# Kernel tuning notes

Measured on AMD Instinct MI355X. Metric: run time of the kernel, lower is better.

## Reference

```python
import jax, jax.numpy as jnp
import numpy as np

D_V, D_Q, D_H = 256, 128, 64

def setup_inputs() -> dict:
    key = jax.random.key(0)
    ks = jax.random.split(key, 8)
    B, T = 512, 512
    query = jax.random.normal(ks[0], (B, D_Q), dtype=jnp.float32)
    values = jax.random.normal(ks[1], (B, T, D_V), dtype=jnp.float32)
    s1 = 1.0 / np.sqrt(D_V)
    s2 = 1.0 / np.sqrt(D_Q)
    sv = 1.0 / np.sqrt(D_H)
    W1 = jax.random.uniform(ks[2], (D_H, D_V), jnp.float32, -s1, s1)
    b1 = jax.random.uniform(ks[3], (D_H,), jnp.float32, -s1, s1)
    W2 = jax.random.uniform(ks[4], (D_H, D_Q), jnp.float32, -s2, s2)
    b2 = jax.random.uniform(ks[5], (D_H,), jnp.float32, -s2, s2)
    Wv = jax.random.uniform(ks[6], (1, D_H), jnp.float32, -sv, sv)
    bv = jax.random.uniform(ks[7], (1,), jnp.float32, -sv, sv)
    return {"query": query, "values": values, "W1": W1, "b1": b1,
            "W2": W2, "b2": b2, "Wv": Wv, "bv": bv}

def reference(query, values, W1, b1, W2, b2, Wv, bv):
    # hidden_with_time_axis: [B,1,128]
    h = jnp.einsum('btv,hv->bth', values, W1) + b1 \
        + (jnp.einsum('bq,hq->bh', query, W2) + b2)[:, None, :]   # [B,T,64]
    score = jnp.einsum('bth,oh->bto', jnp.tanh(h), Wv) + bv        # [B,T,1]
    attention_weights = jax.nn.softmax(score, axis=0)              # softmax over dim 0, as written
    context_vector = jnp.sum(attention_weights * values, axis=0)   # [T,256]
    return (context_vector, attention_weights)
```

## Files before the change

### kernel.cpp

```cpp
#include <hip/hip_runtime.h>
#include <hip/hip_bf16.h>

#define Tt 512
#define Bb 512
#define DV 256
#define DQ 128
#define DH 64
#define CTXN (Tt * DV)

typedef __attribute__((ext_vector_type(8))) short bf16x8;
typedef __attribute__((ext_vector_type(4))) float f32x4;

__device__ __forceinline__ unsigned short f2bf(float x) {
  unsigned u = __float_as_uint(x);
  u += 0x7FFFu + ((u >> 16) & 1u);
  return (unsigned short)(u >> 16);
}

__global__ void qh_kernel(const float* __restrict__ query,
                          const float* __restrict__ W2,
                          const float* __restrict__ b1,
                          const float* __restrict__ b2,
                          float* __restrict__ qh) {
  int b = blockIdx.x;
  int h = threadIdx.x;
  __shared__ float q[DQ];
  q[h]      = query[b * DQ + h];
  q[h + 64] = query[b * DQ + h + 64];
  __syncthreads();
  const float* w2r = W2 + h * DQ;
  float acc = 0.f;
#pragma unroll 8
  for (int k = 0; k < DQ; ++k) acc = fmaf(w2r[k], q[k], acc);
  qh[b * DH + h] = acc + b1[h] + b2[h];
}

__global__ void w1_cvt_kernel(const float* __restrict__ W1,
                              unsigned short* __restrict__ w1bf) {
  int i = blockIdx.x * 256 + threadIdx.x;
  w1bf[i] = f2bf(W1[i]);
}

__global__ __launch_bounds__(256, 2) void score_kernel(
    const float* __restrict__ values,
    const unsigned short* __restrict__ w1bf,
    const float* __restrict__ qh,
    const float* __restrict__ Wv,
    const float* __restrict__ bv,
    float* __restrict__ sT) {
  __shared__ __align__(16) unsigned short lA[64 * DV];
  __shared__ __align__(16) unsigned short lB[DH * DV];
  const int tid = threadIdx.x;
  const int m0 = blockIdx.x * 64;
  const int bidx = m0 >> 9;

  const uint4* w1v = (const uint4*)w1bf;
#pragma unroll
  for (int i = 0; i < 8; ++i) {
    int vec = i * 256 + tid;
    uint4 d = w1v[vec];
    int row = vec >> 5;
    int u = vec & 31;
    int byte = (row << 9) + (u << 4);
    *(uint4*)((char*)lB + (byte ^ ((row & 7) << 4))) = d;
  }
  const float4* vg = (const float4*)values + m0 * (DV / 4);
#pragma unroll
  for (int i = 0; i < 16; ++i) {
    int vec = i * 256 + tid;
    float4 d = vg[vec];
    int row = vec >> 6;
    int c4 = vec & 63;
    uint2 p;
    p.x = (unsigned)f2bf(d.x) | ((unsigned)f2bf(d.y) << 16);
    p.y = (unsigned)f2bf(d.z) | ((unsigned)f2bf(d.w) << 16);
    int byte = (row << 9) + (c4 << 3);
    *(uint2*)((char*)lA + (byte ^ ((row & 7) << 4))) = p;
  }
  __syncthreads();

  const int wv = tid >> 6;
  const int lane = tid & 63;
  const int lrow = lane & 15;
  const int g = lane >> 4;

  f32x4 acc[4];
#pragma unroll
  for (int nt = 0; nt < 4; ++nt) acc[nt] = (f32x4){0.f, 0.f, 0.f, 0.f};

  const int arow = wv * 16 + lrow;
#pragma unroll
  for (int ks = 0; ks < 8; ++ks) {
    int k2 = (ks * 32 + g * 8) * 2;
    int abyte = ((arow << 9) + k2) ^ ((arow & 7) << 4);
    bf16x8 af = *(const bf16x8*)((const char*)lA + abyte);
#pragma unroll
    for (int nt = 0; nt < 4; ++nt) {
      int brow = nt * 16 + lrow;
      bf16x8 bf = *(const bf16x8*)((const char*)lB +
                                   (((brow << 9) + k2) ^ ((brow & 7) << 4)));
      acc[nt] = __builtin_amdgcn_mfma_f32_16x16x32_bf16(af, bf, acc[nt], 0, 0, 0);
    }
  }

  float bv0 = bv[0];
  float sc[4] = {0.f, 0.f, 0.f, 0.f};
#pragma unroll
  for (int nt = 0; nt < 4; ++nt) {
    int col = nt * 16 + lrow;
    float qv = qh[bidx * DH + col];
    float wvc = Wv[col];
#pragma unroll
    for (int j = 0; j < 4; ++j) {
      float hv = acc[nt][j] + qv;
      float e = __expf(2.f * hv);
      float th = (e - 1.f) / (e + 1.f);
      sc[j] = fmaf(th, wvc, sc[j]);
    }
  }
#pragma unroll
  for (int j = 0; j < 4; ++j) {
    float v = sc[j];
    v += __shfl_xor(v, 1);
    v += __shfl_xor(v, 2);
    v += __shfl_xor(v, 4);
    v += __shfl_xor(v, 8);
    sc[j] = v;
  }
  if (lrow == 0) {
#pragma unroll
    for (int j = 0; j < 4; ++j) {
      int m = m0 + wv * 16 + g * 4 + j;
      int tt = m & (Tt - 1);
      sT[tt * Bb + bidx] = sc[j] + bv0;
    }
  }
}

__global__ __launch_bounds__(256) void ctx_kernel(
    const float* __restrict__ values,
    const float* __restrict__ sT,
    float* __restrict__ out) {
  const int t = blockIdx.x;
  const int tid = threadIdx.x;
  const int wv = tid >> 6, lane = tid & 63;
  __shared__ float wbuf[Bb];
  __shared__ float smax[4], ssum[4];
  __shared__ float4 cred[3][64];

  float s0 = sT[t * Bb + tid];
  float s1 = sT[t * Bb + tid + 256];
  float mx = fmaxf(s0, s1);
#pragma unroll
  for (int d = 1; d < 64; d <<= 1) mx = fmaxf(mx, __shfl_xor(mx, d));
  if (lane == 0) smax[wv] = mx;
  __syncthreads();
  mx = fmaxf(fmaxf(smax[0], smax[1]), fmaxf(smax[2], smax[3]));
  float w0 = __expf(s0 - mx), w1 = __expf(s1 - mx);
  float zs = w0 + w1;
#pragma unroll
  for (int d = 1; d < 64; d <<= 1) zs += __shfl_xor(zs, d);
  if (lane == 0) ssum[wv] = zs;
  __syncthreads();
  float invZ = 1.f / (ssum[0] + ssum[1] + ssum[2] + ssum[3]);
  float wn0 = w0 * invZ, wn1 = w1 * invZ;
  wbuf[tid] = wn0;
  wbuf[tid + 256] = wn1;
  out[CTXN + tid * Tt + t] = wn0;
  out[CTXN + (tid + 256) * Tt + t] = wn1;
  __syncthreads();

  const float4* vp = (const float4*)values;
  float4 acc = make_float4(0.f, 0.f, 0.f, 0.f);
#pragma unroll 4
  for (int b = wv; b < Bb; b += 4) {
    float4 v = vp[(size_t)(b * Tt + t) * (DV / 4) + lane];
    float w = wbuf[b];
    acc.x = fmaf(w, v.x, acc.x);
    acc.y = fmaf(w, v.y, acc.y);
    acc.z = fmaf(w, v.z, acc.z);
    acc.w = fmaf(w, v.w, acc.w);
  }
  if (wv > 0) cred[wv - 1][lane] = acc;
  __syncthreads();
  if (wv == 0) {
    float4 a1 = cred[0][lane], a2 = cred[1][lane], a3 = cred[2][lane];
    acc.x += a1.x + a2.x + a3.x;
    acc.y += a1.y + a2.y + a3.y;
    acc.z += a1.z + a2.z + a3.z;
    acc.w += a1.w + a2.w + a3.w;
    ((float4*)out)[t * (DV / 4) + lane] = acc;
  }
}

extern "C" void kernel_launch(void* const* d_in, const int* in_sizes, int n_in,
                              void* d_out, int out_size, void* d_ws, size_t ws_size,
                              hipStream_t stream) {
  const float* query  = (const float*)d_in[0];
  const float* values = (const float*)d_in[1];
  const float* W1     = (const float*)d_in[2];
  const float* b1     = (const float*)d_in[3];
  const float* W2     = (const float*)d_in[4];
  const float* b2     = (const float*)d_in[5];
  const float* Wv     = (const float*)d_in[6];
  const float* bv     = (const float*)d_in[7];
  float* out = (float*)d_out;
  char* ws = (char*)d_ws;
  float* qh            = (float*)ws;
  unsigned short* w1bf = (unsigned short*)(ws + 131072);
  float* sT            = (float*)(ws + 131072 + 32768);

  hipLaunchKernelGGL(qh_kernel, dim3(Bb), dim3(DH), 0, stream, query, W2, b1, b2, qh);
  hipLaunchKernelGGL(w1_cvt_kernel, dim3(64), dim3(256), 0, stream, W1, w1bf);
  hipLaunchKernelGGL(score_kernel, dim3((Bb * Tt) / 64), dim3(256), 0, stream,
                     values, w1bf, qh, Wv, bv, sT);
  hipLaunchKernelGGL(ctx_kernel, dim3(Tt), dim3(256), 0, stream, values, sT, out);
}
```

Before: 102.7 us.

## Load score A-fragments straight from global and widen ctx blocks to 16 waves

The score kernel no longer stages the fp32 values tile into LDS as bf16. Each lane now loads its eight-element A fragment directly from global memory and converts it in registers. This halves the kernel's LDS footprint so launch bounds can request four blocks per CU. The context kernel grows from 256 to 1024 threads, so each of 16 waves accumulates 32 batch rows, which raises memory-level parallelism at the cost of a 16-way LDS reduction at the end.

Result: no change. 103.2 us (+0.5%).

```diff
diff --git a/kernel.cpp b/kernel.cpp
--- a/kernel.cpp
+++ b/kernel.cpp
@@ -41,14 +41,13 @@
   w1bf[i] = f2bf(W1[i]);
 }
 
-__global__ __launch_bounds__(256, 2) void score_kernel(
+__global__ __launch_bounds__(256, 4) void score_kernel(
     const float* __restrict__ values,
     const unsigned short* __restrict__ w1bf,
     const float* __restrict__ qh,
     const float* __restrict__ Wv,
     const float* __restrict__ bv,
     float* __restrict__ sT) {
-  __shared__ __align__(16) unsigned short lA[64 * DV];
   __shared__ __align__(16) unsigned short lB[DH * DV];
   const int tid = threadIdx.x;
   const int m0 = blockIdx.x * 64;
@@ -64,19 +63,6 @@
     int byte = (row << 9) + (u << 4);
     *(uint4*)((char*)lB + (byte ^ ((row & 7) << 4))) = d;
   }
-  const float4* vg = (const float4*)values + m0 * (DV / 4);
-#pragma unroll
-  for (int i = 0; i < 16; ++i) {
-    int vec = i * 256 + tid;
-    float4 d = vg[vec];
-    int row = vec >> 6;
-    int c4 = vec & 63;
-    uint2 p;
-    p.x = (unsigned)f2bf(d.x) | ((unsigned)f2bf(d.y) << 16);
-    p.y = (unsigned)f2bf(d.z) | ((unsigned)f2bf(d.w) << 16);
-    int byte = (row << 9) + (c4 << 3);
-    *(uint2*)((char*)lA + (byte ^ ((row & 7) << 4))) = p;
-  }
   __syncthreads();
 
   const int wv = tid >> 6;
@@ -89,11 +75,19 @@
   for (int nt = 0; nt < 4; ++nt) acc[nt] = (f32x4){0.f, 0.f, 0.f, 0.f};
 
   const int arow = wv * 16 + lrow;
+  const float* ap = values + (size_t)(m0 + arow) * DV;
+
 #pragma unroll
   for (int ks = 0; ks < 8; ++ks) {
+    const float* fp = ap + ks * 32 + g * 8;
+    float4 f0 = *(const float4*)(fp);
+    float4 f1 = *(const float4*)(fp + 4);
+    bf16x8 af;
+    af[0] = (short)f2bf(f0.x); af[1] = (short)f2bf(f0.y);
+    af[2] = (short)f2bf(f0.z); af[3] = (short)f2bf(f0.w);
+    af[4] = (short)f2bf(f1.x); af[5] = (short)f2bf(f1.y);
+    af[6] = (short)f2bf(f1.z); af[7] = (short)f2bf(f1.w);
     int k2 = (ks * 32 + g * 8) * 2;
-    int abyte = ((arow << 9) + k2) ^ ((arow & 7) << 4);
-    bf16x8 af = *(const bf16x8*)((const char*)lA + abyte);
 #pragma unroll
     for (int nt = 0; nt < 4; ++nt) {
       int brow = nt * 16 + lrow;
@@ -137,7 +131,7 @@
   }
 }
 
-__global__ __launch_bounds__(256) void ctx_kernel(
+__global__ __launch_bounds__(1024, 8) void ctx_kernel(
     const float* __restrict__ values,
     const float* __restrict__ sT,
     float* __restrict__ out) {
@@ -145,51 +139,59 @@
   const int tid = threadIdx.x;
   const int wv = tid >> 6, lane = tid & 63;
   __shared__ float wbuf[Bb];
-  __shared__ float smax[4], ssum[4];
-  __shared__ float4 cred[3][64];
-
-  float s0 = sT[t * Bb + tid];
-  float s1 = sT[t * Bb + tid + 256];
-  float mx = fmaxf(s0, s1);
+  __shared__ float smax[16], ssum[16];
+  __shared__ float4 cred[16][64];
+
+  float s = -1e30f;
+  if (tid < Bb) s = sT[t * Bb + tid];
+  float mx = s;
 #pragma unroll
   for (int d = 1; d < 64; d <<= 1) mx = fmaxf(mx, __shfl_xor(mx, d));
   if (lane == 0) smax[wv] = mx;
   __syncthreads();
-  mx = fmaxf(fmaxf(smax[0], smax[1]), fmaxf(smax[2], smax[3]));
-  float w0 = __expf(s0 - mx), w1 = __expf(s1 - mx);
-  float zs = w0 + w1;
+  mx = smax[0];
+#pragma unroll
+  for (int i = 1; i < 16; ++i) mx = fmaxf(mx, smax[i]);
+  float w = (tid < Bb) ? __expf(s - mx) : 0.f;
+  float zs = w;
 #pragma unroll
   for (int d = 1; d < 64; d <<= 1) zs += __shfl_xor(zs, d);
   if (lane == 0) ssum[wv] = zs;
   __syncthreads();
-  float invZ = 1.f / (ssum[0] + ssum[1] + ssum[2] + ssum[3]);
-  float wn0 = w0 * invZ, wn1 = w1 * invZ;
-  wbuf[tid] = wn0;
-  wbuf[tid + 256] = wn1;
-  out[CTXN + tid * Tt + t] = wn0;
-  out[CTXN + (tid + 256) * Tt + t] = wn1;
+  float Z = 0.f;
+#pragma unroll
+  for (int i = 0; i < 16; ++i) Z += ssum[i];
+  float wn = w / Z;
+  if (tid < Bb) {
+    wbuf[tid] = wn;
+    out[CTXN + tid * Tt + t] = wn;
+  }
   __syncthreads();
 
   const float4* vp = (const float4*)values;
+  size_t base = ((size_t)wv * Tt + t) * (DV / 4) + lane;
+  const size_t stride = (size_t)16 * Tt * (DV / 4);
   float4 acc = make_float4(0.f, 0.f, 0.f, 0.f);
 #pragma unroll 4
-  for (int b = wv; b < Bb; b += 4) {
-    float4 v = vp[(size_t)(b * Tt + t) * (DV / 4) + lane];
-    float w = wbuf[b];
-    acc.x = fmaf(w, v.x, acc.x);
-    acc.y = fmaf(w, v.y, acc.y);
-    acc.z = fmaf(w, v.z, acc.z);
-    acc.w = fmaf(w, v.w, acc.w);
-  }
-  if (wv > 0) cred[wv - 1][lane] = acc;
+  for (int i = 0; i < 32; ++i) {
+    float4 v = vp[base];
+    base += stride;
+    float wb = wbuf[wv + (i << 4)];
+    acc.x = fmaf(wb, v.x, acc.x);
+    acc.y = fmaf(wb, v.y, acc.y);
+    acc.z = fmaf(wb, v.z, acc.z);
+    acc.w = fmaf(wb, v.w, acc.w);
+  }
+  cred[wv][lane] = acc;
   __syncthreads();
   if (wv == 0) {
-    float4 a1 = cred[0][lane], a2 = cred[1][lane], a3 = cred[2][lane];
-    acc.x += a1.x + a2.x + a3.x;
-    acc.y += a1.y + a2.y + a3.y;
-    acc.z += a1.z + a2.z + a3.z;
-    acc.w += a1.w + a2.w + a3.w;
-    ((float4*)out)[t * (DV / 4) + lane] = acc;
+    float4 tot = cred[0][lane];
+#pragma unroll
+    for (int i = 1; i < 16; ++i) {
+      float4 a = cred[i][lane];
+      tot.x += a.x; tot.y += a.y; tot.z += a.z; tot.w += a.w;
+    }
+    ((float4*)out)[t * (DV / 4) + lane] = tot;
   }
 }
 
@@ -214,5 +216,5 @@
   hipLaunchKernelGGL(w1_cvt_kernel, dim3(64), dim3(256), 0, stream, W1, w1bf);
   hipLaunchKernelGGL(score_kernel, dim3((Bb * Tt) / 64), dim3(256), 0, stream,
                      values, w1bf, qh, Wv, bv, sT);
-  hipLaunchKernelGGL(ctx_kernel, dim3(Tt), dim3(256), 0, stream, values, sT, out);
-}
+  hipLaunchKernelGGL(ctx_kernel, dim3(Tt), dim3(1024), 0, stream, values, sT, out);
+}
```
